# Kernel optimization log

Hardware: AMD Instinct MI355X
Metric: run time of the kernel (lower is better)

The kernel has to match this reference:

```python
import jax, jax.numpy as jnp
import numpy as np

B, N, C, H = 2, 2048, 1024, 16
D = C // H
NEG = -1e9  # keras Softmax large negative for masked positions


def setup_inputs() -> dict:
    key = jax.random.key(0)
    ks = jax.random.split(key, 10)
    s = lambda fan_in: 1.0 / np.sqrt(fan_in)
    return {
        "x": jax.random.normal(ks[0], (B, N, C), jnp.float32),
        "mask": jnp.ones((B, 1, 1, N), jnp.bool_),
        "Wqkv": jax.random.normal(ks[1], (C, 3 * C), jnp.float32) * s(C),
        "bqkv": jnp.zeros((3 * C,), jnp.float32),
        "Wl": jax.random.normal(ks[2], (H, H), jnp.float32) * s(H),
        "bl": jnp.zeros((H,), jnp.float32),
        "Ww": jax.random.normal(ks[3], (H, H), jnp.float32) * s(H),
        "bw": jnp.zeros((H,), jnp.float32),
        "Wp": jax.random.normal(ks[4], (C, C), jnp.float32) * s(C),
        "bp": jnp.zeros((C,), jnp.float32),
    }


def reference(x, mask, Wqkv, bqkv, Wl, bl, Ww, bw, Wp, bp):
    scale = jnp.asarray(D ** -0.5, x.dtype)
    qkv = x @ Wqkv + bqkv                                  # [B,N,3C]
    qkv = qkv.reshape(B, N, 3, H, D).transpose(2, 0, 3, 1, 4)  # [3,B,H,N,D]
    q, k, v = qkv[0] * scale, qkv[1], qkv[2]
    attn = jnp.einsum("bhnd,bhmd->bhnm", q, k)             # [B,H,N,N]
    # pre-softmax talking-heads: mix head axis
    attn = jnp.einsum("bhnm,hg->bgnm", attn, Wl) + bl[None, :, None, None]
    # keras Softmax with boolean mask: add -1e9 where mask is False
    attn = attn + (1.0 - mask.astype(attn.dtype)) * NEG
    attn = jax.nn.softmax(attn, axis=-1)
    # post-softmax talking-heads
    attn = jnp.einsum("bhnm,hg->bgnm", attn, Ww) + bw[None, :, None, None]
    out = jnp.einsum("bhnm,bhmd->bhnd", attn, v)           # [B,H,N,D]
    out = out.transpose(0, 2, 1, 3).reshape(B, N, C)
    return out @ Wp + bp
```

## Files before the change

### kernel.cpp

```cpp
#include <hip/hip_runtime.h>
#include <hip/hip_bf16.h>


typedef __bf16 bf16_t;
typedef __bf16 bf16x8 __attribute__((ext_vector_type(8)));
typedef float f32x4 __attribute__((ext_vector_type(4)));

#define DEV static __device__ __forceinline__

static constexpr float NEGV = -1e9f;

DEV f32x4 mfma16(bf16x8 a, bf16x8 b, f32x4 c) {
  return __builtin_amdgcn_mfma_f32_16x16x32_bf16(a, b, c, 0, 0, 0);
}

DEV bf16x8 zero8() {
  bf16x8 z;
#pragma unroll
  for (int j = 0; j < 8; ++j) z[j] = (bf16_t)0.0f;
  return z;
}

DEV uint32_t pkbf(float lo, float hi) {
  union { bf16_t f; unsigned short s; } a, b;
  a.f = (bf16_t)lo; b.f = (bf16_t)hi;
  return (uint32_t)a.s | ((uint32_t)b.s << 16);
}

union U84 { uint32_t u[4]; bf16x8 v; };

__global__ __launch_bounds__(256) void mask_prep(const unsigned char* __restrict__ raw,
                                                 unsigned char* __restrict__ canon,
                                                 unsigned char* __restrict__ allflag) {
  __shared__ int c0, c12, f0, f1;
  const int tid = threadIdx.x;
  if (tid == 0) { c0 = 0; c12 = 0; f0 = 1; f1 = 1; }
  __syncthreads();
  int l0 = 0, l12 = 0;
  for (int i = tid; i < 4096; i += 256) {
    unsigned char v = raw[i];
    if (v) {
      int r = i & 3;
      if (r == 0) l0++;
      else if (r < 3) l12++;
    }
  }
  if (l0) atomicAdd(&c0, l0);
  if (l12) atomicAdd(&c12, l12);
  __syncthreads();
  const int mode = (c0 == 0) ? 2 : ((c12 > 0) ? 0 : 1);
  for (int i = tid; i < 4096; i += 256) {
    bool t;
    if (mode == 0)      t = raw[i] != 0;
    else if (mode == 1) t = ((const int*)raw)[i] != 0;
    else                t = ((const float*)raw)[i] != 0.0f;
    canon[i] = t ? 1 : 0;
    if (!t) atomicAnd(i < 2048 ? &f0 : &f1, 0);
  }
  __syncthreads();
  if (tid == 0) { allflag[0] = (unsigned char)f0; allflag[1] = (unsigned char)f1; }
}

__global__ __launch_bounds__(256) void gemm_kernel(
    const float* __restrict__ Af, const bf16_t* __restrict__ Ab,
    const float* __restrict__ Bw, const float* __restrict__ bias,
    float* __restrict__ outf,
    bf16_t* __restrict__ Qs, bf16_t* __restrict__ Ks, bf16_t* __restrict__ Vt,
    int K, int Nn, int epi) {
  __shared__ bf16_t As[64][40];
  __shared__ bf16_t Bs[64][40];
  const int tid = threadIdx.x;
  const int lane = tid & 63, wid = tid >> 6;
  const int bx = blockIdx.x, by = blockIdx.y;
  const int wr = (wid >> 1) * 32, wc = (wid & 1) * 32;
  const int lr = lane & 15, kq = lane >> 4;

  f32x4 acc[2][2];
#pragma unroll
  for (int i = 0; i < 2; ++i)
#pragma unroll
    for (int j = 0; j < 2; ++j) acc[i][j] = (f32x4){0.f, 0.f, 0.f, 0.f};

  for (int kt = 0; kt < K; kt += 32) {
    {
      const int row = tid >> 2, c8 = (tid & 3) * 8;
      if (epi == 0) {
        const float* p = Af + (size_t)(bx * 64 + row) * K + kt + c8;
        float4 v0 = *(const float4*)p;
        float4 v1 = *(const float4*)(p + 4);
        bf16x8 v;
        v[0] = (bf16_t)v0.x; v[1] = (bf16_t)v0.y; v[2] = (bf16_t)v0.z; v[3] = (bf16_t)v0.w;
        v[4] = (bf16_t)v1.x; v[5] = (bf16_t)v1.y; v[6] = (bf16_t)v1.z; v[7] = (bf16_t)v1.w;
        *(bf16x8*)&As[row][c8] = v;
      } else {
        *(bf16x8*)&As[row][c8] =
            *(const bf16x8*)(Ab + (size_t)(bx * 64 + row) * K + kt + c8);
      }
      const int krow = tid >> 3, n8 = (tid & 7) * 8;
      const float* bp = Bw + (size_t)(kt + krow) * Nn + by * 64 + n8;
      float4 b0 = *(const float4*)bp;
      float4 b1 = *(const float4*)(bp + 4);
      Bs[n8 + 0][krow] = (bf16_t)b0.x; Bs[n8 + 1][krow] = (bf16_t)b0.y;
      Bs[n8 + 2][krow] = (bf16_t)b0.z; Bs[n8 + 3][krow] = (bf16_t)b0.w;
      Bs[n8 + 4][krow] = (bf16_t)b1.x; Bs[n8 + 5][krow] = (bf16_t)b1.y;
      Bs[n8 + 6][krow] = (bf16_t)b1.z; Bs[n8 + 7][krow] = (bf16_t)b1.w;
    }
    __syncthreads();
#pragma unroll
    for (int rt = 0; rt < 2; ++rt) {
      bf16x8 af = *(const bf16x8*)&As[wr + rt * 16 + lr][kq * 8];
#pragma unroll
      for (int ct = 0; ct < 2; ++ct) {
        bf16x8 bf = *(const bf16x8*)&Bs[wc + ct * 16 + lr][kq * 8];
        acc[rt][ct] = mfma16(af, bf, acc[rt][ct]);
      }
    }
    __syncthreads();
  }

#pragma unroll
  for (int rt = 0; rt < 2; ++rt)
#pragma unroll
    for (int ct = 0; ct < 2; ++ct)
#pragma unroll
      for (int r = 0; r < 4; ++r) {
        const int grow = bx * 64 + wr + rt * 16 + kq * 4 + r;
        const int gcol = by * 64 + wc + ct * 16 + lr;
        const float v = acc[rt][ct][r] + bias[gcol];
        if (epi == 0) {
          const int t = gcol >> 10, h = (gcol >> 6) & 15, d = gcol & 63;
          const int b = grow >> 11, n = grow & 2047;
          if (t == 0)
            Qs[(((size_t)b * 16 + h) * 2048 + n) * 64 + d] = (bf16_t)(v * 0.125f);
          else if (t == 1)
            Ks[(((size_t)b * 16 + h) * 2048 + n) * 64 + d] = (bf16_t)v;
          else
            Vt[(((size_t)b * 16 + h) * 64 + d) * 2048 + n] = (bf16_t)v;
        } else {
          outf[(size_t)grow * Nn + gcol] = v;
        }
      }
}

__global__ __launch_bounds__(256) void vsum_kernel(const bf16_t* __restrict__ Vt,
                                                   float* __restrict__ Vsum) {
  const int lane = threadIdx.x & 63, wid = threadIdx.x >> 6;
  const int row = blockIdx.x * 4 + wid;
  const bf16_t* p = Vt + (size_t)row * 2048;
  float s = 0.f;
#pragma unroll
  for (int it = 0; it < 4; ++it) {
    bf16x8 v = *(const bf16x8*)(p + it * 512 + lane * 8);
#pragma unroll
    for (int j = 0; j < 8; ++j) s += (float)v[j];
  }
#pragma unroll
  for (int off = 32; off; off >>= 1) s += __shfl_xor(s, off);
  if (lane == 0) Vsum[row] = s;
}

__global__ __launch_bounds__(256, 2) void attn_pass1(
    const bf16_t* __restrict__ Qs, const bf16_t* __restrict__ Ks,
    const unsigned char* __restrict__ canon, const unsigned char* __restrict__ allflag,
    const float* __restrict__ Wl, const float* __restrict__ bl,
    float* __restrict__ pstats) {
  __shared__ uint32_t Sb[5120];
  const int tid = threadIdx.x, lane = tid & 63, wid = tid >> 6;
  const int c = lane & 15, kq = lane >> 4;
  const int job = (blockIdx.x & 7) * 128 + (blockIdx.x >> 3);
  const int mc = job >> 8, b = (job >> 7) & 1, nt = job & 127;
  const int n0 = nt * 16, mbeg = mc * 512;
  const int h0 = 4 * wid;
  const bool allt = allflag[b] != 0;

  bf16x8 wlf;
#pragma unroll
  for (int j = 0; j < 8; ++j) {
    const int k = kq * 8 + j;
    wlf[j] = (k < 16) ? (bf16_t)Wl[k * 16 + c] : (bf16_t)0.0f;
  }
  f32x4 blv;
#pragma unroll
  for (int r = 0; r < 4; ++r) blv[r] = bl[kq * 4 + r];

  bf16x8 qf[4][2];
#pragma unroll
  for (int hh = 0; hh < 4; ++hh)
#pragma unroll
    for (int ks = 0; ks < 2; ++ks)
      qf[hh][ks] = *(const bf16x8*)(Qs + ((size_t)(b * 16 + h0 + hh) * 2048 + n0 + c) *
                                             64 + ks * 32 + kq * 8);

  auto stage = [&](int v) {
    const int m0 = mbeg + v * 32;
#pragma unroll
    for (int hp = 0; hp < 2; ++hp)
#pragma unroll
      for (int mt = 0; mt < 2; ++mt) {
        f32x4 a0 = (f32x4){0.f, 0.f, 0.f, 0.f};
        f32x4 a1 = (f32x4){0.f, 0.f, 0.f, 0.f};
#pragma unroll
        for (int ks = 0; ks < 2; ++ks) {
          bf16x8 k0 = *(const bf16x8*)(Ks + ((size_t)(b * 16 + h0 + hp * 2 + 0) * 2048 +
                                             m0 + mt * 16 + c) * 64 + ks * 32 + kq * 8);
          bf16x8 k1 = *(const bf16x8*)(Ks + ((size_t)(b * 16 + h0 + hp * 2 + 1) * 2048 +
                                             m0 + mt * 16 + c) * 64 + ks * 32 + kq * 8);
          a0 = mfma16(qf[hp * 2 + 0][ks], k0, a0);
          a1 = mfma16(qf[hp * 2 + 1][ks], k1, a1);
        }
#pragma unroll
        for (int r = 0; r < 4; ++r) {
          const int p = (kq * 4 + r) * 32 + mt * 16 + c;
          Sb[p * 10 + ((2 * wid + hp) ^ (kq & 1))] = pkbf(a0[r], a1[r]);
        }
      }
  };

  auto gatherS = [&](int pp) {
    const int prow = (wid * 8 + pp) * 16 + c;
    const int bp = (prow >> 7) & 1;
    if (kq < 2) {
      U84 t;
#pragma unroll
      for (int i = 0; i < 4; ++i) t.u[i] = Sb[prow * 10 + ((kq * 4 + i) ^ bp)];
      return t.v;
    }
    return zero8();
  };

  float lacc[4][4];
#pragma unroll
  for (int r = 0; r < 4; ++r)
#pragma unroll
    for (int ns = 0; ns < 4; ++ns) lacc[r][ns] = 0.f;

  for (int u = 0; u < 16; ++u) {
    stage(u);
    __syncthreads();
#pragma unroll
    for (int pp = 0; pp < 8; ++pp) {
      bf16x8 sf = gatherS(pp);
      f32x4 d1 = mfma16(wlf, sf, blv);
      if (!allt && !canon[b * 2048 + mbeg + u * 32 + (pp & 1) * 16 + c]) {
        d1[0] += NEGV; d1[1] += NEGV; d1[2] += NEGV; d1[3] += NEGV;
      }
      const int ns = pp >> 1;
#pragma unroll
      for (int r = 0; r < 4; ++r) lacc[r][ns] += __expf(d1[r]);
    }
    __syncthreads();
  }

#pragma unroll
  for (int r = 0; r < 4; ++r)
#pragma unroll
    for (int ns = 0; ns < 4; ++ns) {
      float s = lacc[r][ns];
      s += __shfl_xor(s, 1);
      s += __shfl_xor(s, 2);
      s += __shfl_xor(s, 4);
      s += __shfl_xor(s, 8);
      if (c == 0)
        pstats[((size_t)(b * 4 + mc) * 2048 + n0 + wid * 4 + ns) * 16 + kq * 4 + r] = s;
    }
}

__global__ __launch_bounds__(256) void stats_merge(const float* __restrict__ ps,
                                                   float* __restrict__ fin) {
  const int i = blockIdx.x * 256 + threadIdx.x;
  const int b = i >> 15, rest = i & 32767;
  float s = 0.f;
#pragma unroll
  for (int ch = 0; ch < 4; ++ch) s += ps[((size_t)(b * 4 + ch) << 15) + rest];
  fin[i] = 1.0f / s;
}

__global__ __launch_bounds__(256, 2) void attn_pass2(
    const bf16_t* __restrict__ Qs, const bf16_t* __restrict__ Ks,
    const bf16_t* __restrict__ Vt, const unsigned char* __restrict__ canon,
    const unsigned char* __restrict__ allflag,
    const float* __restrict__ Wl, const float* __restrict__ bl,
    const float* __restrict__ Ww, const float* __restrict__ fin,
    float* __restrict__ Opart, int msteps) {
  __shared__ uint32_t Sb[5120];
  __shared__ uint32_t Fb[16 * 260];
  const int tid = threadIdx.x, lane = tid & 63, wid = tid >> 6;
  const int c = lane & 15, kq = lane >> 4;
  const int per = gridDim.x >> 3;
  const int mcN = gridDim.x >> 8;
  const int job = (blockIdx.x & 7) * per + (blockIdx.x >> 3);
  const int mc = job >> 8, b = (job >> 7) & 1, nt = job & 127;
  const int n0 = nt * 16, mbeg = mc * msteps * 32;
  const int h0 = 4 * wid;
  const bool allt = allflag[b] != 0;

  bf16x8 wlf, wwf;
#pragma unroll
  for (int j = 0; j < 8; ++j) {
    const int k = kq * 8 + j;
    wlf[j] = (k < 16) ? (bf16_t)Wl[k * 16 + c] : (bf16_t)0.0f;
    wwf[j] = (k < 16) ? (bf16_t)Ww[k * 16 + c] : (bf16_t)0.0f;
  }
  f32x4 blv;
#pragma unroll
  for (int r = 0; r < 4; ++r) blv[r] = bl[kq * 4 + r];

  float4 ivv[4];
#pragma unroll
  for (int ns = 0; ns < 4; ++ns)
    ivv[ns] =
        *(const float4*)&fin[((size_t)b * 2048 + n0 + wid * 4 + ns) * 16 + kq * 4];

  bf16x8 qf[4][2];
#pragma unroll
  for (int hh = 0; hh < 4; ++hh)
#pragma unroll
    for (int ks = 0; ks < 2; ++ks)
      qf[hh][ks] = *(const bf16x8*)(Qs + ((size_t)(b * 16 + h0 + hh) * 2048 + n0 + c) *
                                             64 + ks * 32 + kq * 8);

  auto stage = [&](int v) {
    const int m0 = mbeg + v * 32;
#pragma unroll
    for (int hp = 0; hp < 2; ++hp)
#pragma unroll
      for (int mt = 0; mt < 2; ++mt) {
        f32x4 a0 = (f32x4){0.f, 0.f, 0.f, 0.f};
        f32x4 a1 = (f32x4){0.f, 0.f, 0.f, 0.f};
#pragma unroll
        for (int ks = 0; ks < 2; ++ks) {
          bf16x8 k0 = *(const bf16x8*)(Ks + ((size_t)(b * 16 + h0 + hp * 2 + 0) * 2048 +
                                             m0 + mt * 16 + c) * 64 + ks * 32 + kq * 8);
          bf16x8 k1 = *(const bf16x8*)(Ks + ((size_t)(b * 16 + h0 + hp * 2 + 1) * 2048 +
                                             m0 + mt * 16 + c) * 64 + ks * 32 + kq * 8);
          a0 = mfma16(qf[hp * 2 + 0][ks], k0, a0);
          a1 = mfma16(qf[hp * 2 + 1][ks], k1, a1);
        }
#pragma unroll
        for (int r = 0; r < 4; ++r) {
          const int p = (kq * 4 + r) * 32 + mt * 16 + c;
          Sb[p * 10 + ((2 * wid + hp) ^ (kq & 1))] = pkbf(a0[r], a1[r]);
        }
      }
  };

  auto gatherS = [&](int pp) {
    const int prow = (wid * 8 + pp) * 16 + c;
    const int bp = (prow >> 7) & 1;
    if (kq < 2) {
      U84 t;
#pragma unroll
      for (int i = 0; i < 4; ++i) t.u[i] = Sb[prow * 10 + ((kq * 4 + i) ^ bp)];
      return t.v;
    }
    return zero8();
  };

  f32x4 oacc[4][4];
#pragma unroll
  for (int i = 0; i < 4; ++i)
#pragma unroll
    for (int j = 0; j < 4; ++j) oacc[i][j] = (f32x4){0.f, 0.f, 0.f, 0.f};

  for (int u = 0; u < msteps; ++u) {
    stage(u);
    __syncthreads();
    bf16_t* fcur = (bf16_t*)Fb;
#pragma unroll
    for (int pp = 0; pp < 8; ++pp) {
      bf16x8 sf = gatherS(pp);
      f32x4 d1 = mfma16(wlf, sf, blv);
      if (!allt && !canon[b * 2048 + mbeg + u * 32 + (pp & 1) * 16 + c]) {
        d1[0] += NEGV; d1[1] += NEGV; d1[2] += NEGV; d1[3] += NEGV;
      }
      const int ns = pp >> 1;
      const float e0 = __expf(d1[0]) * ivv[ns].x;
      const float e1 = __expf(d1[1]) * ivv[ns].y;
      const float e2 = __expf(d1[2]) * ivv[ns].z;
      const float e3 = __expf(d1[3]) * ivv[ns].w;
      const uint32_t Aw = pkbf(e0, e1);
      const uint32_t Bw2 = pkbf(e2, e3);
      const int s0 = (c + 32 * kq) & 63;
      const int s1 = (s0 + 16) & 63;
      U84 ef;
      ef.u[0] = (uint32_t)__shfl((int)Aw, s0);
      ef.u[1] = (uint32_t)__shfl((int)Bw2, s0);
      ef.u[2] = (uint32_t)__shfl((int)Aw, s1);
      ef.u[3] = (uint32_t)__shfl((int)Bw2, s1);
      bf16x8 efv = (kq < 2) ? ef.v : zero8();
      f32x4 d2 = mfma16(wwf, efv, (f32x4){0.f, 0.f, 0.f, 0.f});
      const int pg = wid * 8 + pp;
      const int nl = pg >> 1, ml = (pg & 1) * 16 + c;
      const int wm = (ml >> 1) ^ ((nl & 3) << 2);
#pragma unroll
      for (int r = 0; r < 4; ++r)
        fcur[(kq * 4 + r) * 520 + nl * 32 + wm * 2 + (ml & 1)] = (bf16_t)d2[r];
    }
    __syncthreads();
#pragma unroll
    for (int hh = 0; hh < 4; ++hh) {
      const int g2 = h0 + hh;
      bf16x8 af = *(const bf16x8*)&Fb[g2 * 260 + c * 16 + ((kq ^ (c & 3)) << 2)];
#pragma unroll
      for (int dt = 0; dt < 4; ++dt) {
        bf16x8 vf = *(const bf16x8*)(Vt + ((size_t)(b * 16 + g2) * 64 + dt * 16 + c) *
                                              2048 + mbeg + u * 32 + kq * 8);
        oacc[hh][dt] = mfma16(af, vf, oacc[hh][dt]);
      }
    }
  }

#pragma unroll
  for (int hh = 0; hh < 4; ++hh)
#pragma unroll
    for (int dt = 0; dt < 4; ++dt)
#pragma unroll
      for (int r = 0; r < 4; ++r) {
        const int n = n0 + kq * 4 + r;
        const int col = (h0 + hh) * 64 + dt * 16 + c;
        Opart[(((size_t)b * mcN + mc) * 2048 + n) * 1024 + col] = oacc[hh][dt][r];
      }
}

__global__ __launch_bounds__(256) void reduce_ao(const float* __restrict__ Opart,
                                                 const float* __restrict__ bw,
                                                 const float* __restrict__ Vsum,
                                                 bf16_t* __restrict__ AO, int mcN) {
  const size_t i = ((size_t)blockIdx.x * 256 + threadIdx.x) * 4;
  const int c = (int)(i & 1023), n = (int)((i >> 10) & 2047), b = (int)(i >> 21);
  float vv[4] = {0.f, 0.f, 0.f, 0.f};
  for (int ch = 0; ch < mcN; ++ch) {
    const float4 p =
        *(const float4*)&Opart[(((size_t)b * mcN + ch) * 2048 + n) * 1024 + c];
    vv[0] += p.x; vv[1] += p.y; vv[2] += p.z; vv[3] += p.w;
  }
#pragma unroll
  for (int j = 0; j < 4; ++j) {
    const int cj = c + j, g2 = cj >> 6, d = cj & 63;
    AO[i + j] = (bf16_t)(vv[j] + bw[g2] * Vsum[((size_t)b * 16 + g2) * 64 + d]);
  }
}

extern "C" void kernel_launch(void* const* d_in, const int* in_sizes, int n_in,
                              void* d_out, int out_size, void* d_ws, size_t ws_size,
                              hipStream_t stream) {
  const float* x = (const float*)d_in[0];
  const unsigned char* mask = (const unsigned char*)d_in[1];
  const float* Wqkv = (const float*)d_in[2];
  const float* bqkv = (const float*)d_in[3];
  const float* Wl = (const float*)d_in[4];
  const float* bl = (const float*)d_in[5];
  const float* Ww = (const float*)d_in[6];
  const float* bw = (const float*)d_in[7];
  const float* Wp = (const float*)d_in[8];
  const float* bp = (const float*)d_in[9];
  float* out = (float*)d_out;

  const int mcN = (ws_size >= (size_t)104 * 1024 * 1024) ? 4 : 2;
  const int msteps = 64 / mcN;

  char* w = (char*)d_ws;
  auto alloc = [&](size_t bytes) {
    char* p = w;
    w += (bytes + 255) & ~(size_t)255;
    return p;
  };
  bf16_t* Qs = (bf16_t*)alloc((size_t)2 * 16 * 2048 * 64 * 2);
  bf16_t* Ks = (bf16_t*)alloc((size_t)2 * 16 * 2048 * 64 * 2);
  bf16_t* Vt = (bf16_t*)alloc((size_t)2 * 16 * 2048 * 64 * 2);
  bf16_t* AO = (bf16_t*)alloc((size_t)4096 * 1024 * 2);
  float* Opart = (float*)alloc((size_t)2 * mcN * 2048 * 1024 * 4);
  float* pstats = (float*)alloc((size_t)8 * 2048 * 16 * 4);
  float* fstats = (float*)alloc((size_t)2 * 2048 * 16 * 4);
  float* Vsum = (float*)alloc((size_t)2048 * 4);
  unsigned char* canon = (unsigned char*)alloc(4096);
  unsigned char* allflag = (unsigned char*)alloc(256);

  mask_prep<<<dim3(1), dim3(256), 0, stream>>>(mask, canon, allflag);
  gemm_kernel<<<dim3(64, 48), dim3(256), 0, stream>>>(
      x, (const bf16_t*)nullptr, Wqkv, bqkv, nullptr, Qs, Ks, Vt, 1024, 3072, 0);
  vsum_kernel<<<dim3(512), dim3(256), 0, stream>>>(Vt, Vsum);
  attn_pass1<<<dim3(1024), dim3(256), 0, stream>>>(Qs, Ks, canon, allflag, Wl, bl,
                                                   pstats);
  stats_merge<<<dim3(256), dim3(256), 0, stream>>>(pstats, fstats);
  attn_pass2<<<dim3(mcN * 256), dim3(256), 0, stream>>>(Qs, Ks, Vt, canon, allflag,
                                                        Wl, bl, Ww, fstats, Opart,
                                                        msteps);
  reduce_ao<<<dim3(4096), dim3(256), 0, stream>>>(Opart, bw, Vsum, AO, mcN);
  gemm_kernel<<<dim3(64, 16), dim3(256), 0, stream>>>(
      (const float*)nullptr, AO, Wp, bp, out, nullptr, nullptr, nullptr, 1024, 1024, 1);
}
```

Baseline: 619.6 us.

## Double-buffer LDS in attention pass2 and vectorize S gathers

Pass2 now keeps two LDS buffers for S and for F. The next step's QK staging and the previous step's PV MFMAs are interleaved with the current softmax/mixing work, which removes one barrier per iteration. The S gather in both passes uses 64-bit LDS reads with a per-wave swap in place of four scalar reads. The m-split is also fixed at 2 chunks, which halves the partial-output traffic but lowers grid parallelism. Doubling the LDS footprint may reduce occupancy.

Result: faster. 598.6 us (-3.4%).

```diff
diff --git a/kernel.cpp b/kernel.cpp
--- a/kernel.cpp
+++ b/kernel.cpp
@@ -28,6 +28,17 @@
 }
 
 union U84 { uint32_t u[4]; bf16x8 v; };
+
+DEV bf16x8 gather64(const uint32_t* sb, int prow, int kq, int bp) {
+  if (kq >= 2) return zero8();
+  const uint32_t* base = sb + prow * 10 + kq * 4;
+  const uint2 a = *(const uint2*)base;
+  const uint2 b = *(const uint2*)(base + 2);
+  U84 t;
+  if (bp) { t.u[0] = a.y; t.u[1] = a.x; t.u[2] = b.y; t.u[3] = b.x; }
+  else    { t.u[0] = a.x; t.u[1] = a.y; t.u[2] = b.x; t.u[3] = b.y; }
+  return t.v;
+}
 
 __global__ __launch_bounds__(256) void mask_prep(const unsigned char* __restrict__ raw,
                                                  unsigned char* __restrict__ canon,
@@ -171,6 +182,7 @@
   const int mc = job >> 8, b = (job >> 7) & 1, nt = job & 127;
   const int n0 = nt * 16, mbeg = mc * 512;
   const int h0 = 4 * wid;
+  const int bp = wid & 1;
   const bool allt = allflag[b] != 0;
 
   bf16x8 wlf;
@@ -216,18 +228,6 @@
       }
   };
 
-  auto gatherS = [&](int pp) {
-    const int prow = (wid * 8 + pp) * 16 + c;
-    const int bp = (prow >> 7) & 1;
-    if (kq < 2) {
-      U84 t;
-#pragma unroll
-      for (int i = 0; i < 4; ++i) t.u[i] = Sb[prow * 10 + ((kq * 4 + i) ^ bp)];
-      return t.v;
-    }
-    return zero8();
-  };
-
   float lacc[4][4];
 #pragma unroll
   for (int r = 0; r < 4; ++r)
@@ -239,7 +239,7 @@
     __syncthreads();
 #pragma unroll
     for (int pp = 0; pp < 8; ++pp) {
-      bf16x8 sf = gatherS(pp);
+      bf16x8 sf = gather64(Sb, (wid * 8 + pp) * 16 + c, kq, bp);
       f32x4 d1 = mfma16(wlf, sf, blv);
       if (!allt && !canon[b * 2048 + mbeg + u * 32 + (pp & 1) * 16 + c]) {
         d1[0] += NEGV; d1[1] += NEGV; d1[2] += NEGV; d1[3] += NEGV;
@@ -282,8 +282,8 @@
     const float* __restrict__ Wl, const float* __restrict__ bl,
     const float* __restrict__ Ww, const float* __restrict__ fin,
     float* __restrict__ Opart, int msteps) {
-  __shared__ uint32_t Sb[5120];
-  __shared__ uint32_t Fb[16 * 260];
+  __shared__ uint32_t Sb[2][5120];
+  __shared__ uint32_t Fb[2][16 * 260];
   const int tid = threadIdx.x, lane = tid & 63, wid = tid >> 6;
   const int c = lane & 15, kq = lane >> 4;
   const int per = gridDim.x >> 3;
@@ -292,6 +292,7 @@
   const int mc = job >> 8, b = (job >> 7) & 1, nt = job & 127;
   const int n0 = nt * 16, mbeg = mc * msteps * 32;
   const int h0 = 4 * wid;
+  const int bp = wid & 1;
   const bool allt = allflag[b] != 0;
 
   bf16x8 wlf, wwf;
@@ -319,7 +320,7 @@
       qf[hh][ks] = *(const bf16x8*)(Qs + ((size_t)(b * 16 + h0 + hh) * 2048 + n0 + c) *
                                              64 + ks * 32 + kq * 8);
 
-  auto stage = [&](int v) {
+  auto stage = [&](int v, uint32_t* sb) {
     const int m0 = mbeg + v * 32;
 #pragma unroll
     for (int hp = 0; hp < 2; ++hp)
@@ -339,36 +340,40 @@
 #pragma unroll
         for (int r = 0; r < 4; ++r) {
           const int p = (kq * 4 + r) * 32 + mt * 16 + c;
-          Sb[p * 10 + ((2 * wid + hp) ^ (kq & 1))] = pkbf(a0[r], a1[r]);
+          sb[p * 10 + ((2 * wid + hp) ^ (kq & 1))] = pkbf(a0[r], a1[r]);
         }
       }
   };
 
-  auto gatherS = [&](int pp) {
-    const int prow = (wid * 8 + pp) * 16 + c;
-    const int bp = (prow >> 7) & 1;
-    if (kq < 2) {
-      U84 t;
-#pragma unroll
-      for (int i = 0; i < 4; ++i) t.u[i] = Sb[prow * 10 + ((kq * 4 + i) ^ bp)];
-      return t.v;
-    }
-    return zero8();
-  };
-
   f32x4 oacc[4][4];
 #pragma unroll
   for (int i = 0; i < 4; ++i)
 #pragma unroll
     for (int j = 0; j < 4; ++j) oacc[i][j] = (f32x4){0.f, 0.f, 0.f, 0.f};
 
+  stage(0, Sb[0]);
+  __syncthreads();
   for (int u = 0; u < msteps; ++u) {
-    stage(u);
-    __syncthreads();
-    bf16_t* fcur = (bf16_t*)Fb;
+    const uint32_t* scur = Sb[u & 1];
+    uint32_t* snxt = Sb[(u + 1) & 1];
+    bf16_t* fcur = (bf16_t*)Fb[u & 1];
+    const uint32_t* fprev = Fb[(u + 1) & 1];
+    if (u > 0) {
+#pragma unroll
+      for (int hh = 0; hh < 4; ++hh) {
+        const int g2 = h0 + hh;
+        bf16x8 af = *(const bf16x8*)&fprev[g2 * 260 + c * 16 + ((kq ^ (c & 3)) << 2)];
+#pragma unroll
+        for (int dt = 0; dt < 4; ++dt) {
+          bf16x8 vf = *(const bf16x8*)(Vt + ((size_t)(b * 16 + g2) * 64 + dt * 16 + c) *
+                                                2048 + mbeg + (u - 1) * 32 + kq * 8);
+          oacc[hh][dt] = mfma16(af, vf, oacc[hh][dt]);
+        }
+      }
+    }
 #pragma unroll
     for (int pp = 0; pp < 8; ++pp) {
-      bf16x8 sf = gatherS(pp);
+      bf16x8 sf = gather64(scur, (wid * 8 + pp) * 16 + c, kq, bp);
       f32x4 d1 = mfma16(wlf, sf, blv);
       if (!allt && !canon[b * 2048 + mbeg + u * 32 + (pp & 1) * 16 + c]) {
         d1[0] += NEGV; d1[1] += NEGV; d1[2] += NEGV; d1[3] += NEGV;
@@ -396,15 +401,19 @@
       for (int r = 0; r < 4; ++r)
         fcur[(kq * 4 + r) * 520 + nl * 32 + wm * 2 + (ml & 1)] = (bf16_t)d2[r];
     }
+    if (u < msteps - 1) stage(u + 1, snxt);
     __syncthreads();
+  }
+  {
+    const uint32_t* fprev = Fb[(msteps - 1) & 1];
 #pragma unroll
     for (int hh = 0; hh < 4; ++hh) {
       const int g2 = h0 + hh;
-      bf16x8 af = *(const bf16x8*)&Fb[g2 * 260 + c * 16 + ((kq ^ (c & 3)) << 2)];
+      bf16x8 af = *(const bf16x8*)&fprev[g2 * 260 + c * 16 + ((kq ^ (c & 3)) << 2)];
 #pragma unroll
       for (int dt = 0; dt < 4; ++dt) {
         bf16x8 vf = *(const bf16x8*)(Vt + ((size_t)(b * 16 + g2) * 64 + dt * 16 + c) *
-                                              2048 + mbeg + u * 32 + kq * 8);
+                                              2048 + mbeg + (msteps - 1) * 32 + kq * 8);
         oacc[hh][dt] = mfma16(af, vf, oacc[hh][dt]);
       }
     }
@@ -456,7 +465,7 @@
   const float* bp = (const float*)d_in[9];
   float* out = (float*)d_out;
 
-  const int mcN = (ws_size >= (size_t)104 * 1024 * 1024) ? 4 : 2;
+  const int mcN = 2;
   const int msteps = 64 / mcN;
 
   char* w = (char*)d_ws;
```
